# Kernel tuning notes

Measured on AMD Instinct MI355X. Metric: run time of the kernel, lower is better.

Reference implementation:

```python
import jax, jax.numpy as jnp
import numpy as np

EMBED_DIM = 256
NUM_HEADS = 8
HEAD_DIM = 32
INNER = NUM_HEADS * HEAD_DIM
NEG_SLOPE = 0.2


def setup_inputs() -> dict:
    key = jax.random.key(0)
    ks = jax.random.split(key, 8)
    B, Ns, Nt = 8, 1024, 1024
    src = jax.random.normal(ks[0], (B, Ns, EMBED_DIM), dtype=jnp.float32)
    trg = jax.random.normal(ks[1], (B, Nt, EMBED_DIM), dtype=jnp.float32)
    src_mask = jnp.ones((B, Ns), dtype=bool)
    trg_mask = jax.random.randint(ks[2], (B, Nt), 0, 2).astype(bool)
    # learned params (xavier-ish scale)
    def xavier(k, shape):
        fan_in, fan_out = shape[0], shape[-1]
        lim = (6.0 / (fan_in + fan_out)) ** 0.5
        return jax.random.uniform(k, shape, jnp.float32, -lim, lim)
    W_src = xavier(ks[3], (EMBED_DIM, INNER))
    W_trg = xavier(ks[4], (EMBED_DIM, INNER))  # is_cross_type=True -> independent
    a_src = xavier(ks[5], (NUM_HEADS, HEAD_DIM))
    a_trg = xavier(ks[6], (NUM_HEADS, HEAD_DIM))
    W_out = xavier(ks[7], (INNER, EMBED_DIM))
    return {"src": src, "trg": trg, "src_mask": src_mask, "trg_mask": trg_mask,
            "W_src": W_src, "W_trg": W_trg, "a_src": a_src, "a_trg": a_trg, "W_out": W_out}


def reference(src, trg, src_mask, trg_mask, W_src, W_trg, a_src, a_trg, W_out):
    B, Ns, _ = src.shape
    Nt = trg.shape[1]
    NH, Dh = NUM_HEADS, HEAD_DIM
    src_proj = (src @ W_src).reshape(B, Ns, NH, Dh)  # dropout p=0
    trg_proj = (trg @ W_trg).reshape(B, Nt, NH, Dh)
    score_src = jnp.einsum('bshd,hd->bsh', src_proj, a_src)
    score_trg = jnp.einsum('bthd,hd->bth', trg_proj, a_trg)
    # (B,Ns,NH,1) + (B,1,NH,Nt) -> (B,Ns,NH,Nt)
    scores = score_src[:, :, :, None] + jnp.transpose(score_trg, (0, 2, 1))[:, None, :, :]
    scores = jnp.where(scores >= 0, scores, NEG_SLOPE * scores)  # LeakyReLU
    edge_mask = src_mask[:, :, None, None] & trg_mask[:, None, None, :]
    scores = jnp.where(edge_mask, scores, -jnp.inf)
    attn = jax.nn.softmax(scores, axis=-1)
    attn = jnp.nan_to_num(attn, nan=0.0)
    aggregated = jnp.einsum('bsht,bthd->bshd', attn, trg_proj)
    output = aggregated.reshape(B, Ns, NH * Dh) @ W_out
    return output, jnp.transpose(attn, (0, 2, 1, 3))
```

## Files before the change

### kernel.cpp

```cpp
#include <hip/hip_runtime.h>
#include <hip/hip_bf16.h>
#include <math.h>

#define NB 8
#define NS 1024
#define NT 1024
#define NE 256
#define NHEADS 8
#define DH 32
#define LOG2E 1.4426950408889634f

typedef __attribute__((ext_vector_type(8))) short short8;
typedef __attribute__((ext_vector_type(8))) unsigned short ushort8;
typedef __attribute__((ext_vector_type(4))) float f32x4;

#define O_VT    0u
#define O_WTT   (8u<<20)
#define O_WTO   ((8u<<20)+131072u)
#define O_CSRC  ((8u<<20)+262144u)
#define O_CTRG  (O_CSRC+8192u)
#define O_SSRC  (O_CTRG+8192u)
#define O_STRG  (O_SSRC+262144u)
#define O_FLAG  (O_STRG+262144u)
#define O_EST   (12u<<20)

__device__ __forceinline__ unsigned short f2bf(float f) {
    __hip_bfloat16 h = __float2bfloat16(f);
    union { __hip_bfloat16 h; unsigned short u; } c; c.h = h;
    return c.u;
}
__device__ __forceinline__ float leaky(float v) {
    return (v >= 0.f) ? v : 0.2f * v;
}
__device__ __forceinline__ float exp2_fast(float x) {
    float r;
    asm("v_exp_f32 %0, %1" : "=v"(r) : "v"(x));
    return r;
}

__global__ __launch_bounds__(256) void setup_kernel(
    const unsigned* __restrict__ tmask_dw, const float* __restrict__ Wsrc,
    const float* __restrict__ Wtrg, const float* __restrict__ Wout,
    const float* __restrict__ asrc, const float* __restrict__ atrg,
    float* __restrict__ c_src, float* __restrict__ c_trg,
    unsigned short* __restrict__ Wt_t, unsigned short* __restrict__ Wt_o,
    int* __restrict__ flag) {
    __shared__ __align__(16) char sm[16640];
    const int tid = threadIdx.x;
    const int bid = blockIdx.x;

    if (bid == 0) {
        __shared__ int s_ok;
        if (tid == 0) s_ok = 1;
        __syncthreads();
        for (int i = tid; i < 2048; i += 256)
            if (tmask_dw[i] > 1u) s_ok = 0;
        __syncthreads();
        if (tid == 0) *flag = s_ok;
    } else if (bid <= 2) {
        float* a_sh = (float*)sm;
        const float* W = (bid == 1) ? Wsrc : Wtrg;
        const float* a = (bid == 1) ? asrc : atrg;
        float* c = (bid == 1) ? c_src : c_trg;
        a_sh[tid] = a[tid];
        __syncthreads();
        const int e = tid;
        float ch[8];
#pragma unroll
        for (int h = 0; h < 8; ++h) ch[h] = 0.f;
        for (int i = 0; i < 64; ++i) {
            const float4 wv = *(const float4*)&W[(size_t)e * NE + i * 4];
            const int h = i >> 3, d0 = (i & 7) * 4;
            ch[h] += wv.x * a_sh[h * 32 + d0] + wv.y * a_sh[h * 32 + d0 + 1] +
                     wv.z * a_sh[h * 32 + d0 + 2] + wv.w * a_sh[h * 32 + d0 + 3];
        }
#pragma unroll
        for (int h = 0; h < 8; ++h) c[h * NE + e] = ch[h];
    } else {
        const int q = bid - 3;
        const float* W = (q >> 4) ? Wout : Wtrg;
        unsigned short* Wt = (q >> 4) ? Wt_o : Wt_t;
        const int tl = q & 15;
        const int k0 = (tl >> 2) * 64, n0 = (tl & 3) * 64;
        float* xs = (float*)sm;
#pragma unroll
        for (int it = 0; it < 4; ++it) {
            const int slot = it * 256 + tid;
            const int k = slot >> 4, c4 = slot & 15;
            const float4 v = *(const float4*)&W[(size_t)(k0 + k) * NE + n0 + c4 * 4];
            float* p = &xs[k * 65 + c4 * 4];
            p[0] = v.x; p[1] = v.y; p[2] = v.z; p[3] = v.w;
        }
        __syncthreads();
#pragma unroll
        for (int it = 0; it < 2; ++it) {
            const int slot = it * 256 + tid;
            const int n = slot >> 3, kc = slot & 7;
            ushort8 v;
#pragma unroll
            for (int e = 0; e < 8; ++e)
                v[e] = f2bf(xs[(kc * 8 + e) * 65 + n]);
            *(ushort8*)&Wt[(size_t)(n0 + n) * NE + k0 + kc * 8] = v;
        }
    }
}

__global__ __launch_bounds__(256) void mid_kernel(
    const float* __restrict__ src, const float* __restrict__ trg,
    const float* __restrict__ c_src, const float* __restrict__ c_trg,
    const unsigned short* __restrict__ Wt_t, unsigned short* __restrict__ Vt,
    float* __restrict__ ssrc, float* __restrict__ strg,
    const void* __restrict__ tmask, const int* __restrict__ flag_p,
    float2* __restrict__ estg) {
    __shared__ __align__(16) char sm[49152];
    const int tid = threadIdx.x;
    const int bid = blockIdx.x;

    if (bid < 256) {
        unsigned short* As = (unsigned short*)sm;
        unsigned short* ldsT = (unsigned short*)(sm + 32768);
        const int lane = tid & 63, w = tid >> 6;
        const int row0 = (bid >> 1) * 64;
        const int col0 = (bid & 1) * 128;

#pragma unroll
        for (int it = 0; it < 8; ++it) {
            const int gf = it * 256 + tid;
            const int row = gf >> 5, g3 = gf & 31;
            const float4 a = *(const float4*)&trg[(size_t)(row0 + row) * NE + g3 * 8];
            const float4 b = *(const float4*)&trg[(size_t)(row0 + row) * NE + g3 * 8 + 4];
            ushort8 v;
            v[0] = f2bf(a.x); v[1] = f2bf(a.y); v[2] = f2bf(a.z); v[3] = f2bf(a.w);
            v[4] = f2bf(b.x); v[5] = f2bf(b.y); v[6] = f2bf(b.z); v[7] = f2bf(b.w);
            *(ushort8*)&As[row * NE + ((g3 ^ (row & 7)) * 8)] = v;
        }
        __syncthreads();

        const int r = lane & 15, g = lane >> 4;
        short8 af[8];
#pragma unroll
        for (int kk = 0; kk < 8; ++kk)
            af[kk] = *(const short8*)&As[(w * 16 + r) * NE + (((kk * 4 + g) ^ (r & 7)) * 8)];

        f32x4 acc[8];
#pragma unroll
        for (int nt = 0; nt < 8; ++nt) acc[nt] = (f32x4){0.f, 0.f, 0.f, 0.f};
#pragma unroll
        for (int kk = 0; kk < 8; ++kk) {
#pragma unroll
            for (int nt = 0; nt < 8; ++nt) {
                const int col = col0 + nt * 16 + r;
                const short8 bf = *(const short8*)&Wt_t[(size_t)col * NE + kk * 32 + g * 8];
                acc[nt] = __builtin_amdgcn_mfma_f32_16x16x32_bf16(af[kk], bf, acc[nt], 0, 0, 0);
            }
        }
        __syncthreads();

#pragma unroll
        for (int nt = 0; nt < 8; ++nt) {
            const int cl = nt * 16 + r;
            const int sw = (cl & 7) << 3;
#pragma unroll
            for (int j = 0; j < 4; ++j) {
                const int t = w * 16 + g * 4 + j;
                ldsT[cl * 64 + (t ^ sw)] = f2bf(acc[nt][j]);
            }
        }
        __syncthreads();

        const int b = row0 >> 10, t0 = row0 & 1023;
#pragma unroll
        for (int it = 0; it < 4; ++it) {
            const int slot = it * 256 + tid;
            const int cl = slot >> 3, ch = slot & 7;
            const int colg = col0 + cl;
            const int h = colg >> 5, d = colg & 31;
            *(ushort8*)&Vt[(((size_t)(b * 8 + h)) * 32 + d) * 1024 + t0 + ch * 8] =
                *(const ushort8*)&ldsT[cl * 64 + ch * 8];
        }
    } else {
        float* xs = (float*)sm;
        float* cs = (float*)(sm + 32768);
        const int rowg0 = (bid - 256) * 32;
        const bool is_src = rowg0 < NB * NS;
        const float* X = is_src ? (src + (size_t)rowg0 * NE)
                                : (trg + (size_t)(rowg0 - NB * NS) * NE);
        const float* C = is_src ? c_src : c_trg;
        float* S = is_src ? (ssrc + (size_t)rowg0 * NHEADS)
                          : (strg + (size_t)(rowg0 - NB * NS) * NHEADS);

#pragma unroll
        for (int it = 0; it < 8; ++it) {
            const int slot = it * 256 + tid;
            const int row = slot >> 6, c4 = slot & 63;
            *(float4*)&xs[row * NE + c4 * 4] =
                *(const float4*)&X[(size_t)row * NE + c4 * 4];
            cs[slot] = C[slot];
        }
        __syncthreads();

        const int r = tid >> 3, h = tid & 7;
        float s = 0.f;
        for (int e = 0; e < NE; e += 4) {
            const float4 x = *(const float4*)&xs[r * NE + e];
            const float4 c = *(const float4*)&cs[h * NE + e];
            s += x.x * c.x + x.y * c.y + x.z * c.z + x.w * c.w;
        }
        S[(size_t)r * NHEADS + h] = s;

        if (!is_src) {
            const int rowg = rowg0 - NB * NS + r;
            const int flag = *flag_p;
            const bool mv = flag ? (((const int*)tmask)[rowg] != 0)
                                 : (((const unsigned char*)tmask)[rowg] != 0);
            const int bb = rowg >> 10, tt = rowg & 1023;
            const float s2 = s * LOG2E;
            float2 e;
            e.x = mv ? exp2_fast(s2) : 0.f;
            e.y = mv ? exp2_fast(0.2f * s2) : 0.f;
            estg[(size_t)(bb * 8 + h) * 1024 + tt] = e;
        }
    }
}

__global__ __launch_bounds__(512) void combo_kernel(
    const float* __restrict__ ssrc, const float* __restrict__ strg,
    const void* __restrict__ smask, const void* __restrict__ tmask,
    const int* __restrict__ flag_p, const unsigned short* __restrict__ Vt,
    const unsigned short* __restrict__ Wt_o, const float2* __restrict__ estg,
    float* __restrict__ attn, float* __restrict__ out) {
    __shared__ __align__(16) char sm[41472];
    const int bid = blockIdx.x;
    const int tid = threadIdx.x;
    const int lane = tid & 63;
    const int w = tid >> 6;
    const int flag = *flag_p;

    const int fam = (bid >> 3) & 1;
    const int idx = (bid & 7) | ((bid >> 4) << 3);

    if (fam == 0) {
        const int q = idx & 63;
        const int b = idx >> 6;
        float* s_sm = (float*)sm;
        unsigned short* agg_sw = (unsigned short*)(sm + 32768);
        float* s_inv = (float*)(sm + 32768 + 8192);

        for (int t = tid; t < NT; t += 512) {
            const bool mv = flag ? (((const int*)tmask)[b * NT + t] != 0)
                                 : (((const unsigned char*)tmask)[b * NT + t] != 0);
            const float4 s0 = *(const float4*)&strg[((size_t)b * NT + t) * 8];
            const float4 s1 = *(const float4*)&strg[((size_t)b * NT + t) * 8 + 4];
            const float sv[8] = {s0.x, s0.y, s0.z, s0.w, s1.x, s1.y, s1.z, s1.w};
#pragma unroll
            for (int h = 0; h < 8; ++h)
                s_sm[h * 1024 + t] = mv ? sv[h] * LOG2E : -1e30f;
        }
        __syncthreads();

        const int r = lane & 15;
        const int g = lane >> 4;
        const int srow = q * 16 + r;
        const bool rowv = flag ? (((const int*)smask)[b * NS + srow] != 0)
                               : (((const unsigned char*)smask)[b * NS + srow] != 0);
        const int sw = (r & 7) << 3;
        const int h = w;
        const float ss2 = ssrc[((size_t)b * NS + srow) * NHEADS + h] * LOG2E;
        const unsigned short* vr0 = Vt + (size_t)(b * 8 + h) * 32768 + r * 1024;
        const unsigned short* vr1 = vr0 + 16 * 1024;

        f32x4 acc0 = {0.f, 0.f, 0.f, 0.f};
        f32x4 acc1 = {0.f, 0.f, 0.f, 0.f};
        float sum = 0.f;
#pragma unroll 4
        for (int c = 0; c < 32; ++c) {
            const int tb = c * 32 + g * 8;
            const short8 b0 = *(const short8*)&vr0[tb ^ sw];
            const short8 b1 = *(const short8*)&vr1[tb ^ sw];
            const float4 v0 = *(const float4*)&s_sm[h * 1024 + tb];
            const float4 v1 = *(const float4*)&s_sm[h * 1024 + tb + 4];
            const float vv[8] = {v0.x, v0.y, v0.z, v0.w, v1.x, v1.y, v1.z, v1.w};
            short8 pa;
#pragma unroll
            for (int e = 0; e < 8; ++e) {
                const float p = exp2_fast(leaky(ss2 + vv[e]));
                sum += p;
                pa[e] = (short)f2bf(p);
            }
            acc0 = __builtin_amdgcn_mfma_f32_16x16x32_bf16(pa, b0, acc0, 0, 0, 0);
            acc1 = __builtin_amdgcn_mfma_f32_16x16x32_bf16(pa, b1, acc1, 0, 0, 0);
        }
        sum += __shfl_xor(sum, 16);
        sum += __shfl_xor(sum, 32);
        const float inv = (rowv && sum > 0.f) ? 1.f / sum : 0.f;
        if (g == 0) s_inv[h * 16 + r] = inv;
        __syncthreads();

#pragma unroll
        for (int j = 0; j < 4; ++j) {
            const int row = g * 4 + j;
            const float iv = s_inv[h * 16 + row];
            int col = h * 32 + r;
            agg_sw[row * 256 + ((((col >> 3) ^ (row & 7)) << 3) | (col & 7))] =
                f2bf(acc0[j] * iv);
            col += 16;
            agg_sw[row * 256 + ((((col >> 3) ^ (row & 7)) << 3) | (col & 7))] =
                f2bf(acc1[j] * iv);
        }
        __syncthreads();

        f32x4 oacc[2];
#pragma unroll
        for (int nt = 0; nt < 2; ++nt) oacc[nt] = (f32x4){0.f, 0.f, 0.f, 0.f};
#pragma unroll
        for (int kk = 0; kk < 8; ++kk) {
            const short8 af = *(const short8*)&agg_sw[r * 256 + (((kk * 4 + g) ^ (r & 7)) * 8)];
#pragma unroll
            for (int nt = 0; nt < 2; ++nt) {
                const int col = w * 32 + nt * 16 + r;
                const short8 bf = *(const short8*)&Wt_o[(size_t)col * NE + kk * 32 + g * 8];
                oacc[nt] = __builtin_amdgcn_mfma_f32_16x16x32_bf16(af, bf, oacc[nt], 0, 0, 0);
            }
        }
#pragma unroll
        for (int nt = 0; nt < 2; ++nt) {
            const int col = w * 32 + nt * 16 + r;
#pragma unroll
            for (int j = 0; j < 4; ++j)
                out[((size_t)b * NS + q * 16 + g * 4 + j) * NE + col] = oacc[nt][j];
        }
    } else {
        const int b = idx >> 6;
        const int h = (idx >> 3) & 7;
        const int hq = idx & 7;

        float2 e[16];
        const float2* eb = estg + (size_t)(b * 8 + h) * 1024;
#pragma unroll
        for (int qq = 0; qq < 4; ++qq) {
            const float4 p0 = *(const float4*)&eb[qq * 256 + lane * 4];
            const float4 p1 = *(const float4*)&eb[qq * 256 + lane * 4 + 2];
            e[qq * 4 + 0] = make_float2(p0.x, p0.y);
            e[qq * 4 + 1] = make_float2(p0.z, p0.w);
            e[qq * 4 + 2] = make_float2(p1.x, p1.y);
            e[qq * 4 + 3] = make_float2(p1.z, p1.w);
        }

        const int row0 = hq * 128 + w * 16;
        for (int rr = 0; rr < 16; ++rr) {
            const int srow = row0 + rr;
            const float ss2 = ssrc[((size_t)b * NS + srow) * NHEADS + h] * LOG2E;
            const bool rowv = flag ? (((const int*)smask)[b * NS + srow] != 0)
                                   : (((const unsigned char*)smask)[b * NS + srow] != 0);
            const float e1 = exp2_fast(ss2);
            const float e2 = exp2_fast(0.2f * ss2);
            const float thr = exp2_fast(-ss2);

            float sum = 0.f;
#pragma unroll
            for (int k = 0; k < 16; ++k)
                sum += (e[k].x >= thr) ? e[k].x * e1 : e[k].y * e2;
#pragma unroll
            for (int off = 32; off >= 1; off >>= 1)
                sum += __shfl_xor(sum, off);
            const float inv = (rowv && sum > 0.f) ? 1.f / sum : 0.f;
            const float v1 = e1 * inv, v2 = e2 * inv;

            float* arow = attn + ((size_t)(b * NHEADS + h) * NS + srow) * NT;
#pragma unroll
            for (int qq = 0; qq < 4; ++qq) {
                float4 o;
                o.x = (e[qq * 4 + 0].x >= thr) ? e[qq * 4 + 0].x * v1 : e[qq * 4 + 0].y * v2;
                o.y = (e[qq * 4 + 1].x >= thr) ? e[qq * 4 + 1].x * v1 : e[qq * 4 + 1].y * v2;
                o.z = (e[qq * 4 + 2].x >= thr) ? e[qq * 4 + 2].x * v1 : e[qq * 4 + 2].y * v2;
                o.w = (e[qq * 4 + 3].x >= thr) ? e[qq * 4 + 3].x * v1 : e[qq * 4 + 3].y * v2;
                *(float4*)&arow[qq * 256 + lane * 4] = o;
            }
        }
    }
}

extern "C" void kernel_launch(void* const* d_in, const int* in_sizes, int n_in,
                              void* d_out, int out_size, void* d_ws, size_t ws_size,
                              hipStream_t stream) {
    const float* src   = (const float*)d_in[0];
    const float* trg   = (const float*)d_in[1];
    const void*  smask = d_in[2];
    const void*  tmask = d_in[3];
    const float* Wsrc  = (const float*)d_in[4];
    const float* Wtrg  = (const float*)d_in[5];
    const float* asrc  = (const float*)d_in[6];
    const float* atrg  = (const float*)d_in[7];
    const float* Wout  = (const float*)d_in[8];

    float* out  = (float*)d_out;
    float* attn = out + (size_t)NB * NS * NE;

    char* wsb = (char*)d_ws;
    unsigned short* Vt   = (unsigned short*)(wsb + O_VT);
    unsigned short* Wt_t = (unsigned short*)(wsb + O_WTT);
    unsigned short* Wt_o = (unsigned short*)(wsb + O_WTO);
    float* c_src = (float*)(wsb + O_CSRC);
    float* c_trg = (float*)(wsb + O_CTRG);
    float* ssrc  = (float*)(wsb + O_SSRC);
    float* strg  = (float*)(wsb + O_STRG);
    int*   flag  = (int*)(wsb + O_FLAG);
    float2* estg = (float2*)(wsb + O_EST);

    setup_kernel<<<35, 256, 0, stream>>>(
        (const unsigned*)tmask, Wsrc, Wtrg, Wout, asrc, atrg,
        c_src, c_trg, Wt_t, Wt_o, flag);

    mid_kernel<<<768, 256, 0, stream>>>(
        src, trg, c_src, c_trg, Wt_t, Vt, ssrc, strg, tmask, flag, estg);

    combo_kernel<<<1024, 512, 0, stream>>>(
        ssrc, strg, smask, tmask, flag, Vt, Wt_o, estg, attn, out);
}
```

Before: 93.52 us.

## Process 32 source rows per aggregation block to reuse V and Wout fragments

Each aggregation block in the combined kernel now handles two 16-row source tiles instead of one. The V-transpose fragments, the shared target scores and the Wout fragments are loaded once and fed to twice as many MFMAs, which halves the global and L2 traffic per output row for that block family. The grid shrinks from 1024 to 768 blocks, interleaved one aggregation block to two attention-write blocks. Shared memory is cut by aliasing the aggregation buffer over the score buffer. The cost is higher register pressure from doubled accumulators and fewer aggregation blocks to spread across CUs.

```diff
diff --git a/kernel.cpp b/kernel.cpp
--- a/kernel.cpp
+++ b/kernel.cpp
@@ -229,22 +229,22 @@
     const int* __restrict__ flag_p, const unsigned short* __restrict__ Vt,
     const unsigned short* __restrict__ Wt_o, const float2* __restrict__ estg,
     float* __restrict__ attn, float* __restrict__ out) {
-    __shared__ __align__(16) char sm[41472];
+    __shared__ __align__(16) char sm[33792];
     const int bid = blockIdx.x;
     const int tid = threadIdx.x;
     const int lane = tid & 63;
     const int w = tid >> 6;
     const int flag = *flag_p;
 
-    const int fam = (bid >> 3) & 1;
-    const int idx = (bid & 7) | ((bid >> 4) << 3);
+    const int fam = (bid % 3 == 0) ? 0 : 1;
+    const int idx = (fam == 0) ? (bid / 3) : (bid - bid / 3 - 1);
 
     if (fam == 0) {
-        const int q = idx & 63;
-        const int b = idx >> 6;
+        const int q32 = idx & 31;
+        const int b = idx >> 5;
         float* s_sm = (float*)sm;
-        unsigned short* agg_sw = (unsigned short*)(sm + 32768);
-        float* s_inv = (float*)(sm + 32768 + 8192);
+        unsigned short* agg_sw = (unsigned short*)sm;
+        float* s_inv = (float*)(sm + 32768);
 
         for (int t = tid; t < NT; t += 512) {
             const bool mv = flag ? (((const int*)tmask)[b * NT + t] != 0)
@@ -260,19 +260,23 @@
 
         const int r = lane & 15;
         const int g = lane >> 4;
-        const int srow = q * 16 + r;
-        const bool rowv = flag ? (((const int*)smask)[b * NS + srow] != 0)
-                               : (((const unsigned char*)smask)[b * NS + srow] != 0);
+        const int h = w;
         const int sw = (r & 7) << 3;
-        const int h = w;
-        const float ss2 = ssrc[((size_t)b * NS + srow) * NHEADS + h] * LOG2E;
+        const int srowA = q32 * 32 + r;
+        const int srowB = srowA + 16;
+        const bool rowvA = flag ? (((const int*)smask)[b * NS + srowA] != 0)
+                                : (((const unsigned char*)smask)[b * NS + srowA] != 0);
+        const bool rowvB = flag ? (((const int*)smask)[b * NS + srowB] != 0)
+                                : (((const unsigned char*)smask)[b * NS + srowB] != 0);
+        const float ssA = ssrc[((size_t)b * NS + srowA) * NHEADS + h] * LOG2E;
+        const float ssB = ssrc[((size_t)b * NS + srowB) * NHEADS + h] * LOG2E;
         const unsigned short* vr0 = Vt + (size_t)(b * 8 + h) * 32768 + r * 1024;
         const unsigned short* vr1 = vr0 + 16 * 1024;
 
-        f32x4 acc0 = {0.f, 0.f, 0.f, 0.f};
-        f32x4 acc1 = {0.f, 0.f, 0.f, 0.f};
-        float sum = 0.f;
-#pragma unroll 4
+        f32x4 acc0A = {0.f, 0.f, 0.f, 0.f}, acc1A = {0.f, 0.f, 0.f, 0.f};
+        f32x4 acc0B = {0.f, 0.f, 0.f, 0.f}, acc1B = {0.f, 0.f, 0.f, 0.f};
+        float sumA = 0.f, sumB = 0.f;
+#pragma unroll 2
         for (int c = 0; c < 32; ++c) {
             const int tb = c * 32 + g * 8;
             const short8 b0 = *(const short8*)&vr0[tb ^ sw];
@@ -280,54 +284,76 @@
             const float4 v0 = *(const float4*)&s_sm[h * 1024 + tb];
             const float4 v1 = *(const float4*)&s_sm[h * 1024 + tb + 4];
             const float vv[8] = {v0.x, v0.y, v0.z, v0.w, v1.x, v1.y, v1.z, v1.w};
-            short8 pa;
+            short8 paA, paB;
 #pragma unroll
             for (int e = 0; e < 8; ++e) {
-                const float p = exp2_fast(leaky(ss2 + vv[e]));
-                sum += p;
-                pa[e] = (short)f2bf(p);
+                const float pA = exp2_fast(leaky(ssA + vv[e]));
+                const float pB = exp2_fast(leaky(ssB + vv[e]));
+                sumA += pA;
+                sumB += pB;
+                paA[e] = (short)f2bf(pA);
+                paB[e] = (short)f2bf(pB);
             }
-            acc0 = __builtin_amdgcn_mfma_f32_16x16x32_bf16(pa, b0, acc0, 0, 0, 0);
-            acc1 = __builtin_amdgcn_mfma_f32_16x16x32_bf16(pa, b1, acc1, 0, 0, 0);
-        }
-        sum += __shfl_xor(sum, 16);
-        sum += __shfl_xor(sum, 32);
-        const float inv = (rowv && sum > 0.f) ? 1.f / sum : 0.f;
-        if (g == 0) s_inv[h * 16 + r] = inv;
+            acc0A = __builtin_amdgcn_mfma_f32_16x16x32_bf16(paA, b0, acc0A, 0, 0, 0);
+            acc1A = __builtin_amdgcn_mfma_f32_16x16x32_bf16(paA, b1, acc1A, 0, 0, 0);
+            acc0B = __builtin_amdgcn_mfma_f32_16x16x32_bf16(paB, b0, acc0B, 0, 0, 0);
+            acc1B = __builtin_amdgcn_mfma_f32_16x16x32_bf16(paB, b1, acc1B, 0, 0, 0);
+        }
+        sumA += __shfl_xor(sumA, 16);
+        sumA += __shfl_xor(sumA, 32);
+        sumB += __shfl_xor(sumB, 16);
+        sumB += __shfl_xor(sumB, 32);
+        const float invA = (rowvA && sumA > 0.f) ? 1.f / sumA : 0.f;
+        const float invB = (rowvB && sumB > 0.f) ? 1.f / sumB : 0.f;
+        if (g == 0) {
+            s_inv[h * 32 + r] = invA;
+            s_inv[h * 32 + 16 + r] = invB;
+        }
         __syncthreads();
 
 #pragma unroll
         for (int j = 0; j < 4; ++j) {
-            const int row = g * 4 + j;
-            const float iv = s_inv[h * 16 + row];
+            const int rowA = g * 4 + j;
+            const int rowB = 16 + g * 4 + j;
+            const float ivA = s_inv[h * 32 + rowA];
+            const float ivB = s_inv[h * 32 + rowB];
             int col = h * 32 + r;
-            agg_sw[row * 256 + ((((col >> 3) ^ (row & 7)) << 3) | (col & 7))] =
-                f2bf(acc0[j] * iv);
+            agg_sw[rowA * 256 + ((((col >> 3) ^ (rowA & 7)) << 3) | (col & 7))] =
+                f2bf(acc0A[j] * ivA);
+            agg_sw[rowB * 256 + ((((col >> 3) ^ (rowB & 7)) << 3) | (col & 7))] =
+                f2bf(acc0B[j] * ivB);
             col += 16;
-            agg_sw[row * 256 + ((((col >> 3) ^ (row & 7)) << 3) | (col & 7))] =
-                f2bf(acc1[j] * iv);
-        }
-        __syncthreads();
-
-        f32x4 oacc[2];
-#pragma unroll
-        for (int nt = 0; nt < 2; ++nt) oacc[nt] = (f32x4){0.f, 0.f, 0.f, 0.f};
+            agg_sw[rowA * 256 + ((((col >> 3) ^ (rowA & 7)) << 3) | (col & 7))] =
+                f2bf(acc1A[j] * ivA);
+            agg_sw[rowB * 256 + ((((col >> 3) ^ (rowB & 7)) << 3) | (col & 7))] =
+                f2bf(acc1B[j] * ivB);
+        }
+        __syncthreads();
+
+        f32x4 oacc0A = {0.f, 0.f, 0.f, 0.f}, oacc1A = {0.f, 0.f, 0.f, 0.f};
+        f32x4 oacc0B = {0.f, 0.f, 0.f, 0.f}, oacc1B = {0.f, 0.f, 0.f, 0.f};
 #pragma unroll
         for (int kk = 0; kk < 8; ++kk) {
-            const short8 af = *(const short8*)&agg_sw[r * 256 + (((kk * 4 + g) ^ (r & 7)) * 8)];
-#pragma unroll
-            for (int nt = 0; nt < 2; ++nt) {
-                const int col = w * 32 + nt * 16 + r;
-                const short8 bf = *(const short8*)&Wt_o[(size_t)col * NE + kk * 32 + g * 8];
-                oacc[nt] = __builtin_amdgcn_mfma_f32_16x16x32_bf16(af, bf, oacc[nt], 0, 0, 0);
+            const short8 afA = *(const short8*)&agg_sw[r * 256 + (((kk * 4 + g) ^ (r & 7)) * 8)];
+            const short8 afB = *(const short8*)&agg_sw[(16 + r) * 256 + (((kk * 4 + g) ^ (r & 7)) * 8)];
+            const int col0 = w * 32 + r;
+            const short8 bf0 = *(const short8*)&Wt_o[(size_t)col0 * NE + kk * 32 + g * 8];
+            const short8 bf1 = *(const short8*)&Wt_o[(size_t)(col0 + 16) * NE + kk * 32 + g * 8];
+            oacc0A = __builtin_amdgcn_mfma_f32_16x16x32_bf16(afA, bf0, oacc0A, 0, 0, 0);
+            oacc1A = __builtin_amdgcn_mfma_f32_16x16x32_bf16(afA, bf1, oacc1A, 0, 0, 0);
+            oacc0B = __builtin_amdgcn_mfma_f32_16x16x32_bf16(afB, bf0, oacc0B, 0, 0, 0);
+            oacc1B = __builtin_amdgcn_mfma_f32_16x16x32_bf16(afB, bf1, oacc1B, 0, 0, 0);
+        }
+        {
+            const int colA = w * 32 + r;
+            float* ob = out + ((size_t)b * NS + q32 * 32 + g * 4) * NE;
+#pragma unroll
+            for (int j = 0; j < 4; ++j) {
+                ob[(size_t)j * NE + colA] = oacc0A[j];
+                ob[(size_t)j * NE + colA + 16] = oacc1A[j];
+                ob[(size_t)(16 + j) * NE + colA] = oacc0B[j];
+                ob[(size_t)(16 + j) * NE + colA + 16] = oacc1B[j];
             }
-        }
-#pragma unroll
-        for (int nt = 0; nt < 2; ++nt) {
-            const int col = w * 32 + nt * 16 + r;
-#pragma unroll
-            for (int j = 0; j < 4; ++j)
-                out[((size_t)b * NS + q * 16 + g * 4 + j) * NE + col] = oacc[nt][j];
         }
     } else {
         const int b = idx >> 6;
@@ -414,6 +440,6 @@
     mid_kernel<<<768, 256, 0, stream>>>(
         src, trg, c_src, c_trg, Wt_t, Vt, ssrc, strg, tmask, flag, estg);
 
-    combo_kernel<<<1024, 512, 0, stream>>>(
+    combo_kernel<<<768, 512, 0, stream>>>(
         ssrc, strg, smask, tmask, flag, Vt, Wt_o, estg, attn, out);
 }
```

Result: slower. 96.38 us (+3.1%).

## Co-schedule aggregation and attention-writer waves in one block with pre-transposed scores

Applied to the files above, without the earlier changes.

The combo kernel now launches 512 blocks of 1024 threads instead of 1024 blocks of 512. In each block, eight waves run the aggregation and output GEMM for one (batch, 16-row) tile. The other eight waves write the attention rows for the same tile, one head per wave. The mid kernel also writes a head-major, log2-scaled and masked copy of the target scores. Each aggregation wave copies only its own head's slice into LDS, so the full-block staging loop, the mask reads and one barrier go away. The barrier pairing between the two wave groups now depends on barriers in divergent branches matching up. Larger blocks may also reduce scheduling flexibility.

```diff
diff --git a/kernel.cpp b/kernel.cpp
--- a/kernel.cpp
+++ b/kernel.cpp
@@ -23,6 +23,7 @@
 #define O_STRG  (O_SSRC+262144u)
 #define O_FLAG  (O_STRG+262144u)
 #define O_EST   (12u<<20)
+#define O_STRGT (13u<<20)
 
 __device__ __forceinline__ unsigned short f2bf(float f) {
     __hip_bfloat16 h = __float2bfloat16(f);
@@ -111,7 +112,7 @@
     const unsigned short* __restrict__ Wt_t, unsigned short* __restrict__ Vt,
     float* __restrict__ ssrc, float* __restrict__ strg,
     const void* __restrict__ tmask, const int* __restrict__ flag_p,
-    float2* __restrict__ estg) {
+    float2* __restrict__ estg, float* __restrict__ strgT) {
     __shared__ __align__(16) char sm[49152];
     const int tid = threadIdx.x;
     const int bid = blockIdx.x;
@@ -219,53 +220,48 @@
             e.x = mv ? exp2_fast(s2) : 0.f;
             e.y = mv ? exp2_fast(0.2f * s2) : 0.f;
             estg[(size_t)(bb * 8 + h) * 1024 + tt] = e;
+            strgT[(size_t)(bb * 8 + h) * 1024 + tt] = mv ? s2 : -1e30f;
         }
     }
 }
 
-__global__ __launch_bounds__(512) void combo_kernel(
-    const float* __restrict__ ssrc, const float* __restrict__ strg,
-    const void* __restrict__ smask, const void* __restrict__ tmask,
+__global__ __launch_bounds__(1024) void combo_kernel(
+    const float* __restrict__ ssrc, const float* __restrict__ strgT,
+    const void* __restrict__ smask,
     const int* __restrict__ flag_p, const unsigned short* __restrict__ Vt,
     const unsigned short* __restrict__ Wt_o, const float2* __restrict__ estg,
     float* __restrict__ attn, float* __restrict__ out) {
-    __shared__ __align__(16) char sm[41472];
+    __shared__ __align__(16) float s_sm[8 * 1024];
+    __shared__ __align__(16) unsigned short agg_sw[16 * 256];
+    __shared__ float s_inv[128];
     const int bid = blockIdx.x;
     const int tid = threadIdx.x;
     const int lane = tid & 63;
     const int w = tid >> 6;
     const int flag = *flag_p;
 
-    const int fam = (bid >> 3) & 1;
-    const int idx = (bid & 7) | ((bid >> 4) << 3);
-
-    if (fam == 0) {
-        const int q = idx & 63;
-        const int b = idx >> 6;
-        float* s_sm = (float*)sm;
-        unsigned short* agg_sw = (unsigned short*)(sm + 32768);
-        float* s_inv = (float*)(sm + 32768 + 8192);
-
-        for (int t = tid; t < NT; t += 512) {
-            const bool mv = flag ? (((const int*)tmask)[b * NT + t] != 0)
-                                 : (((const unsigned char*)tmask)[b * NT + t] != 0);
-            const float4 s0 = *(const float4*)&strg[((size_t)b * NT + t) * 8];
-            const float4 s1 = *(const float4*)&strg[((size_t)b * NT + t) * 8 + 4];
-            const float sv[8] = {s0.x, s0.y, s0.z, s0.w, s1.x, s1.y, s1.z, s1.w};
-#pragma unroll
-            for (int h = 0; h < 8; ++h)
-                s_sm[h * 1024 + t] = mv ? sv[h] * LOG2E : -1e30f;
-        }
-        __syncthreads();
-
+    const int q = bid & 63;
+    const int b = bid >> 6;
+
+    if (w < 8) {
+        const int h = w;
         const int r = lane & 15;
         const int g = lane >> 4;
         const int srow = q * 16 + r;
         const bool rowv = flag ? (((const int*)smask)[b * NS + srow] != 0)
                                : (((const unsigned char*)smask)[b * NS + srow] != 0);
         const int sw = (r & 7) << 3;
-        const int h = w;
         const float ss2 = ssrc[((size_t)b * NS + srow) * NHEADS + h] * LOG2E;
+
+        {
+            const float* st = strgT + (size_t)(b * 8 + h) * 1024;
+#pragma unroll
+            for (int it = 0; it < 4; ++it) {
+                const int t4 = it * 256 + lane * 4;
+                *(float4*)&s_sm[h * 1024 + t4] = *(const float4*)&st[t4];
+            }
+        }
+
         const unsigned short* vr0 = Vt + (size_t)(b * 8 + h) * 32768 + r * 1024;
         const unsigned short* vr1 = vr0 + 16 * 1024;
 
@@ -294,7 +290,6 @@
         sum += __shfl_xor(sum, 32);
         const float inv = (rowv && sum > 0.f) ? 1.f / sum : 0.f;
         if (g == 0) s_inv[h * 16 + r] = inv;
-        __syncthreads();
 
 #pragma unroll
         for (int j = 0; j < 4; ++j) {
@@ -330,9 +325,7 @@
                 out[((size_t)b * NS + q * 16 + g * 4 + j) * NE + col] = oacc[nt][j];
         }
     } else {
-        const int b = idx >> 6;
-        const int h = (idx >> 3) & 7;
-        const int hq = idx & 7;
+        const int h = w - 8;
 
         float2 e[16];
         const float2* eb = estg + (size_t)(b * 8 + h) * 1024;
@@ -346,7 +339,7 @@
             e[qq * 4 + 3] = make_float2(p1.z, p1.w);
         }
 
-        const int row0 = hq * 128 + w * 16;
+        const int row0 = q * 16;
         for (int rr = 0; rr < 16; ++rr) {
             const int srow = row0 + rr;
             const float ss2 = ssrc[((size_t)b * NS + srow) * NHEADS + h] * LOG2E;
@@ -377,6 +370,7 @@
                 *(float4*)&arow[qq * 256 + lane * 4] = o;
             }
         }
+        __syncthreads();
     }
 }
 
@@ -406,14 +400,15 @@
     float* strg  = (float*)(wsb + O_STRG);
     int*   flag  = (int*)(wsb + O_FLAG);
     float2* estg = (float2*)(wsb + O_EST);
+    float* strgT = (float*)(wsb + O_STRGT);
 
     setup_kernel<<<35, 256, 0, stream>>>(
         (const unsigned*)tmask, Wsrc, Wtrg, Wout, asrc, atrg,
         c_src, c_trg, Wt_t, Wt_o, flag);
 
     mid_kernel<<<768, 256, 0, stream>>>(
-        src, trg, c_src, c_trg, Wt_t, Vt, ssrc, strg, tmask, flag, estg);
-
-    combo_kernel<<<1024, 512, 0, stream>>>(
-        ssrc, strg, smask, tmask, flag, Vt, Wt_o, estg, attn, out);
-}
+        src, trg, c_src, c_trg, Wt_t, Vt, ssrc, strg, tmask, flag, estg, strgT);
+
+    combo_kernel<<<512, 1024, 0, stream>>>(
+        ssrc, strgT, smask, flag, Vt, Wt_o, estg, attn, out);
+}
```

Result: slower. 97.85 us (+4.6%).
